# Kernel tuning notes

Hardware: AMD Instinct MI355X
Metric: run time of the kernel (lower is better)

The kernel has to match this reference:

```python
import jax, jax.numpy as jnp
import numpy as np

B, V, DIM = 64, 64, 512
H = 2 * DIM  # 1024 hidden units


def setup_inputs() -> dict:
    key = jax.random.key(0)
    ks = jax.random.split(key, 7)
    scale = 0.05
    return {
        "state": jax.random.normal(ks[0], (B, DIM), jnp.float32),
        "action": jax.random.normal(ks[1], (B, DIM), jnp.float32),
        "embed": jax.random.normal(ks[2], (V, DIM), jnp.float32),
        "W1": jax.random.normal(ks[3], (3 * DIM, H), jnp.float32) * scale,
        "b1": jax.random.normal(ks[4], (H,), jnp.float32) * scale,
        "W2": jax.random.normal(ks[5], (H, 1), jnp.float32) * scale,
        "b2": jax.random.normal(ks[6], (1,), jnp.float32) * scale,
    }


def reference(state, action, embed, W1, b1, W2, b2):
    # Original torch code concatenates [cause, effect, ctx] along the feature
    # dim then applies Linear(3*dim, 2*dim). Equivalently, split W1 into three
    # [dim, 2*dim] blocks and sum the three small matmuls (avoids materializing
    # the [B,V,V,3*dim] concat tensor).
    Wc, We, Wx = W1[:DIM], W1[DIM:2 * DIM], W1[2 * DIM:]
    cause_h = embed @ Wc                   # [V, H]
    effect_h = embed @ We                  # [V, H]
    ctx_h = (state + action) @ Wx          # [B, H]
    # broadcast-sum -> [B, V, V, H]
    h = ctx_h[:, None, None, :] + cause_h[None, :, None, :] + effect_h[None, None, :, :] + b1
    h = jax.nn.gelu(h, approximate=False)  # torch nn.GELU default is exact erf
    logits = jnp.einsum("bijh,ho->bij", h, W2) + b2[0]  # [B, V, V]
    scores = jax.nn.sigmoid(logits).mean(axis=0)        # [V, V]
    return scores
```

## Files before the change

kernel.cpp:

```cpp
#include <hip/hip_runtime.h>

#define DIM 512
#define HH  1024
#define NB  64
#define NV  64


static __device__ __forceinline__ float fast_gelu(float x) {
    const float C1 = -0.0713548162f * 1.4426950408889634f;
    const float C0 = -1.5957691216f * 1.4426950408889634f;
    float x2 = x * x;
    float u  = x * fmaf(C1, x2, C0);
    float e  = __builtin_amdgcn_exp2f(u);
    return x * __builtin_amdgcn_rcpf(1.0f + e);
}

extern "C" __global__ __launch_bounds__(256)
void cgl_prep(const float* __restrict__ state, const float* __restrict__ action,
              const float* __restrict__ embed, const float* __restrict__ W1,
              const float* __restrict__ b1, float* __restrict__ ws)
{
    __shared__ float arow[4][DIM];
    const int m   = blockIdx.x >> 4;
    const int rg  = blockIdx.x & 15;
    const int tid = threadIdx.x;

    for (int idx = tid; idx < 4 * DIM; idx += 256) {
        int r = idx >> 9, k = idx & (DIM - 1);
        int row = rg * 4 + r;
        float v = (m == 2) ? (state[row * DIM + k] + action[row * DIM + k])
                           : embed[row * DIM + k];
        arow[r][k] = v;
    }
    __syncthreads();

    const float* Wm = W1 + m * DIM * HH;
    const int c = tid * 4;
    float4 acc0 = {0,0,0,0}, acc1 = {0,0,0,0}, acc2 = {0,0,0,0}, acc3 = {0,0,0,0};
    for (int k = 0; k < DIM; ++k) {
        const float4 w = *reinterpret_cast<const float4*>(Wm + k * HH + c);
        float a0 = arow[0][k], a1 = arow[1][k], a2 = arow[2][k], a3 = arow[3][k];
        acc0.x = fmaf(a0, w.x, acc0.x); acc0.y = fmaf(a0, w.y, acc0.y);
        acc0.z = fmaf(a0, w.z, acc0.z); acc0.w = fmaf(a0, w.w, acc0.w);
        acc1.x = fmaf(a1, w.x, acc1.x); acc1.y = fmaf(a1, w.y, acc1.y);
        acc1.z = fmaf(a1, w.z, acc1.z); acc1.w = fmaf(a1, w.w, acc1.w);
        acc2.x = fmaf(a2, w.x, acc2.x); acc2.y = fmaf(a2, w.y, acc2.y);
        acc2.z = fmaf(a2, w.z, acc2.z); acc2.w = fmaf(a2, w.w, acc2.w);
        acc3.x = fmaf(a3, w.x, acc3.x); acc3.y = fmaf(a3, w.y, acc3.y);
        acc3.z = fmaf(a3, w.z, acc3.z); acc3.w = fmaf(a3, w.w, acc3.w);
    }

    float* ctx   = ws;
    float* cause = ws + NB * HH;
    float* effT  = ws + 2 * NB * HH;
    float4 accs[4] = {acc0, acc1, acc2, acc3};
    if (m == 0) {
        #pragma unroll
        for (int r = 0; r < 4; ++r)
            *reinterpret_cast<float4*>(cause + (rg * 4 + r) * HH + c) = accs[r];
    } else if (m == 1) {
        #pragma unroll
        for (int r = 0; r < 4; ++r) {
            int row = rg * 4 + r;
            effT[(c + 0) * NV + row] = accs[r].x;
            effT[(c + 1) * NV + row] = accs[r].y;
            effT[(c + 2) * NV + row] = accs[r].z;
            effT[(c + 3) * NV + row] = accs[r].w;
        }
    } else {
        const float4 bv = *reinterpret_cast<const float4*>(b1 + c);
        #pragma unroll
        for (int r = 0; r < 4; ++r) {
            float4 o = accs[r];
            o.x += bv.x; o.y += bv.y; o.z += bv.z; o.w += bv.w;
            *reinterpret_cast<float4*>(ctx + (rg * 4 + r) * HH + c) = o;
        }
    }
}

extern "C" __global__ __launch_bounds__(256)
void cgl_score(const float* __restrict__ ws, const float* __restrict__ W2,
               const float* __restrict__ b2, float* __restrict__ out)
{
    __shared__ float pre[4][HH];
    __shared__ float w2s[HH];
    __shared__ float eff[64][64];
    __shared__ float red[4][64];

    const float* ctx   = ws;
    const float* cause = ws + NB * HH;
    const float* effT  = ws + 2 * NB * HH;

    const int i    = blockIdx.x & 63;
    const int bg   = blockIdx.x >> 6;
    const int tid  = threadIdx.x;
    const int wave = tid >> 6;
    const int lane = tid & 63;

    for (int idx = tid; idx < 4 * HH; idx += 256) {
        int w = idx >> 10, h = idx & (HH - 1);
        pre[w][h] = ctx[(bg * 4 + w) * HH + h] + cause[i * HH + h];
    }
    for (int h = tid; h < HH; h += 256) w2s[h] = W2[h];

    float acc = 0.0f;
    for (int hc = 0; hc < 16; ++hc) {
        __syncthreads();
        {
            const float4* src = reinterpret_cast<const float4*>(effT + hc * 64 * 64);
            float4* dst = reinterpret_cast<float4*>(&eff[0][0]);
            for (int idx = tid; idx < 1024; idx += 256) dst[idx] = src[idx];
        }
        __syncthreads();
        #pragma unroll
        for (int dh = 0; dh < 64; ++dh) {
            const int h = hc * 64 + dh;
            float x = pre[wave][h] + eff[dh][lane];
            acc = fmaf(fast_gelu(x), w2s[h], acc);
        }
    }

    float logit = acc + b2[0];
    float s = __builtin_amdgcn_rcpf(
        1.0f + __builtin_amdgcn_exp2f(-1.4426950408889634f * logit));
    red[wave][lane] = s;
    __syncthreads();
    if (wave == 0) {
        float r = (red[0][lane] + red[1][lane] + red[2][lane] + red[3][lane])
                  * (1.0f / 64.0f);
        atomicAdd(&out[i * 64 + lane], r);
    }
}

extern "C" void kernel_launch(void* const* d_in, const int* in_sizes, int n_in,
                              void* d_out, int out_size, void* d_ws, size_t ws_size,
                              hipStream_t stream) {
    const float* state  = (const float*)d_in[0];
    const float* action = (const float*)d_in[1];
    const float* embed  = (const float*)d_in[2];
    const float* W1     = (const float*)d_in[3];
    const float* b1     = (const float*)d_in[4];
    const float* W2     = (const float*)d_in[5];
    const float* b2     = (const float*)d_in[6];
    float* ws = (float*)d_ws;

    hipMemsetAsync(d_out, 0, out_size * sizeof(float), stream);
    cgl_prep<<<48, 256, 0, stream>>>(state, action, embed, W1, b1, ws);
    cgl_score<<<64 * 16, 256, 0, stream>>>(ws, W2, b2, (float*)d_out);
}
```

Measured before the change: 216.2 us.

## Split prep GEMM over K with atomics and split score hidden dim across waves

The prep kernel now splits the K dimension into 8 chunks, launching 384 blocks instead of 48, and accumulates partial results with atomicAdd into a workspace that is zeroed first. The score kernel uses 512 threads per block, with two wave groups each covering half of the hidden dimension, and combines their partial logits before the sigmoid. The aim is to fill more compute units in the underused prep stage and raise occupancy in the score stage. In exchange it adds a workspace memset, many scalar atomics and a nondeterministic summation order.

```diff
diff --git a/kernel.cpp b/kernel.cpp
--- a/kernel.cpp
+++ b/kernel.cpp
@@ -20,26 +20,27 @@
               const float* __restrict__ embed, const float* __restrict__ W1,
               const float* __restrict__ b1, float* __restrict__ ws)
 {
-    __shared__ float arow[4][DIM];
-    const int m   = blockIdx.x >> 4;
-    const int rg  = blockIdx.x & 15;
+    __shared__ float arow[4][64];
+    const int m   = blockIdx.x >> 7;
+    const int rg  = (blockIdx.x >> 3) & 15;
+    const int kc  = blockIdx.x & 7;
     const int tid = threadIdx.x;
 
-    for (int idx = tid; idx < 4 * DIM; idx += 256) {
-        int r = idx >> 9, k = idx & (DIM - 1);
-        int row = rg * 4 + r;
-        float v = (m == 2) ? (state[row * DIM + k] + action[row * DIM + k])
-                           : embed[row * DIM + k];
-        arow[r][k] = v;
+    {
+        int r = tid >> 6, kk = tid & 63;
+        int row = rg * 4 + r, k = kc * 64 + kk;
+        arow[r][kk] = (m == 2) ? (state[row * DIM + k] + action[row * DIM + k])
+                               : embed[row * DIM + k];
     }
     __syncthreads();
 
-    const float* Wm = W1 + m * DIM * HH;
+    const float* Wm = W1 + m * DIM * HH + kc * 64 * HH;
     const int c = tid * 4;
     float4 acc0 = {0,0,0,0}, acc1 = {0,0,0,0}, acc2 = {0,0,0,0}, acc3 = {0,0,0,0};
-    for (int k = 0; k < DIM; ++k) {
-        const float4 w = *reinterpret_cast<const float4*>(Wm + k * HH + c);
-        float a0 = arow[0][k], a1 = arow[1][k], a2 = arow[2][k], a3 = arow[3][k];
+    #pragma unroll 4
+    for (int kk = 0; kk < 64; ++kk) {
+        const float4 w = *reinterpret_cast<const float4*>(Wm + kk * HH + c);
+        float a0 = arow[0][kk], a1 = arow[1][kk], a2 = arow[2][kk], a3 = arow[3][kk];
         acc0.x = fmaf(a0, w.x, acc0.x); acc0.y = fmaf(a0, w.y, acc0.y);
         acc0.z = fmaf(a0, w.z, acc0.z); acc0.w = fmaf(a0, w.w, acc0.w);
         acc1.x = fmaf(a1, w.x, acc1.x); acc1.y = fmaf(a1, w.y, acc1.y);
@@ -54,38 +55,42 @@
     float* cause = ws + NB * HH;
     float* effT  = ws + 2 * NB * HH;
     float4 accs[4] = {acc0, acc1, acc2, acc3};
-    if (m == 0) {
-        #pragma unroll
-        for (int r = 0; r < 4; ++r)
-            *reinterpret_cast<float4*>(cause + (rg * 4 + r) * HH + c) = accs[r];
-    } else if (m == 1) {
-        #pragma unroll
-        for (int r = 0; r < 4; ++r) {
-            int row = rg * 4 + r;
-            effT[(c + 0) * NV + row] = accs[r].x;
-            effT[(c + 1) * NV + row] = accs[r].y;
-            effT[(c + 2) * NV + row] = accs[r].z;
-            effT[(c + 3) * NV + row] = accs[r].w;
-        }
-    } else {
+
+    if (m == 2 && kc == 0) {
         const float4 bv = *reinterpret_cast<const float4*>(b1 + c);
         #pragma unroll
         for (int r = 0; r < 4; ++r) {
-            float4 o = accs[r];
-            o.x += bv.x; o.y += bv.y; o.z += bv.z; o.w += bv.w;
-            *reinterpret_cast<float4*>(ctx + (rg * 4 + r) * HH + c) = o;
+            accs[r].x += bv.x; accs[r].y += bv.y;
+            accs[r].z += bv.z; accs[r].w += bv.w;
+        }
+    }
+
+    #pragma unroll
+    for (int r = 0; r < 4; ++r) {
+        const int row = rg * 4 + r;
+        if (m == 1) {
+            atomicAdd(&effT[(c + 0) * NV + row], accs[r].x);
+            atomicAdd(&effT[(c + 1) * NV + row], accs[r].y);
+            atomicAdd(&effT[(c + 2) * NV + row], accs[r].z);
+            atomicAdd(&effT[(c + 3) * NV + row], accs[r].w);
+        } else {
+            float* base = ((m == 0) ? cause : ctx) + row * HH + c;
+            atomicAdd(base + 0, accs[r].x);
+            atomicAdd(base + 1, accs[r].y);
+            atomicAdd(base + 2, accs[r].z);
+            atomicAdd(base + 3, accs[r].w);
         }
     }
 }
 
-extern "C" __global__ __launch_bounds__(256)
+extern "C" __global__ __launch_bounds__(512, 8)
 void cgl_score(const float* __restrict__ ws, const float* __restrict__ W2,
                const float* __restrict__ b2, float* __restrict__ out)
 {
     __shared__ float pre[4][HH];
+    __shared__ float eff[2][32][64];
     __shared__ float w2s[HH];
-    __shared__ float eff[64][64];
-    __shared__ float red[4][64];
+    __shared__ float red[8][64];
 
     const float* ctx   = ws;
     const float* cause = ws + NB * HH;
@@ -96,39 +101,40 @@
     const int tid  = threadIdx.x;
     const int wave = tid >> 6;
     const int lane = tid & 63;
+    const int bq   = wave & 3;
+    const int hh   = wave >> 2;
 
-    for (int idx = tid; idx < 4 * HH; idx += 256) {
+    for (int idx = tid; idx < 4 * HH; idx += 512) {
         int w = idx >> 10, h = idx & (HH - 1);
         pre[w][h] = ctx[(bg * 4 + w) * HH + h] + cause[i * HH + h];
     }
-    for (int h = tid; h < HH; h += 256) w2s[h] = W2[h];
+    for (int h = tid; h < HH; h += 512) w2s[h] = W2[h];
 
     float acc = 0.0f;
-    for (int hc = 0; hc < 16; ++hc) {
+    const int base_h = hh * 512;
+    for (int c = 0; c < 16; ++c) {
         __syncthreads();
-        {
-            const float4* src = reinterpret_cast<const float4*>(effT + hc * 64 * 64);
-            float4* dst = reinterpret_cast<float4*>(&eff[0][0]);
-            for (int idx = tid; idx < 1024; idx += 256) dst[idx] = src[idx];
+        for (int idx = tid; idx < 1024; idx += 512) {
+            int q = idx >> 9, r = idx & 511;
+            reinterpret_cast<float4*>(&eff[q][0][0])[r] =
+                reinterpret_cast<const float4*>(effT + (q * 512 + c * 32) * NV)[r];
         }
         __syncthreads();
         #pragma unroll
-        for (int dh = 0; dh < 64; ++dh) {
-            const int h = hc * 64 + dh;
-            float x = pre[wave][h] + eff[dh][lane];
+        for (int dh = 0; dh < 32; ++dh) {
+            const int h = base_h + c * 32 + dh;
+            float x = pre[bq][h] + eff[hh][dh][lane];
             acc = fmaf(fast_gelu(x), w2s[h], acc);
         }
     }
 
-    float logit = acc + b2[0];
-    float s = __builtin_amdgcn_rcpf(
-        1.0f + __builtin_amdgcn_exp2f(-1.4426950408889634f * logit));
-    red[wave][lane] = s;
+    red[wave][lane] = acc;
     __syncthreads();
-    if (wave == 0) {
-        float r = (red[0][lane] + red[1][lane] + red[2][lane] + red[3][lane])
-                  * (1.0f / 64.0f);
-        atomicAdd(&out[i * 64 + lane], r);
+    if (wave < 4) {
+        float logit = red[wave][lane] + red[wave + 4][lane] + b2[0];
+        float s = __builtin_amdgcn_rcpf(
+            1.0f + __builtin_amdgcn_exp2f(-1.4426950408889634f * logit));
+        atomicAdd(&out[i * 64 + lane], s * (1.0f / 64.0f));
     }
 }
 
@@ -145,6 +151,7 @@
     float* ws = (float*)d_ws;
 
     hipMemsetAsync(d_out, 0, out_size * sizeof(float), stream);
-    cgl_prep<<<48, 256, 0, stream>>>(state, action, embed, W1, b1, ws);
-    cgl_score<<<64 * 16, 256, 0, stream>>>(ws, W2, b2, (float*)d_out);
+    hipMemsetAsync(d_ws, 0, 3 * NB * HH * sizeof(float), stream);
+    cgl_prep<<<384, 256, 0, stream>>>(state, action, embed, W1, b1, ws);
+    cgl_score<<<64 * 16, 512, 0, stream>>>(ws, W2, b2, (float*)d_out);
 }
```

Result: faster. 201.7 us (-6.7%).
